# Optimization experiments

Hardware: AMD Instinct MI355X
Metric: run time of the kernel (lower is better)

The kernel has to match this reference:

```python
import jax, jax.numpy as jnp
import numpy as np

N_NODES = 50000


def _sage_max(x, src, dst, W_l, b_l, W_r):
    # gather neighbor (source) features, scatter-max to destination nodes
    msgs = x[src]                                   # [E, F]
    agg = jax.ops.segment_max(msgs, dst, num_segments=N_NODES)  # [N, F], -inf for empty
    agg = jnp.where(jnp.isneginf(agg), 0.0, agg)    # PyG fills isolated nodes with 0
    return agg @ W_l + b_l + x @ W_r                # lin_l(aggr) + lin_r(x)


def setup_inputs() -> dict:
    key = jax.random.key(0)
    ks = jax.random.split(key, 9)
    F_IN, H, OUT, E, EL = 128, 256, 32, 800000, 200000
    x = jax.random.normal(ks[0], (N_NODES, F_IN), dtype=jnp.float32)
    edge_index = jax.random.randint(ks[1], (2, E), 0, N_NODES, dtype=jnp.int64)
    edge_label_index = jax.random.randint(ks[2], (2, EL), 0, N_NODES, dtype=jnp.int64)
    s1 = 1.0 / np.sqrt(F_IN)
    s2 = 1.0 / np.sqrt(H)
    W1_l = jax.random.normal(ks[3], (F_IN, H), dtype=jnp.float32) * s1
    b1 = jnp.zeros((H,), dtype=jnp.float32)
    W1_r = jax.random.normal(ks[4], (F_IN, H), dtype=jnp.float32) * s1
    W2_l = jax.random.normal(ks[5], (H, OUT), dtype=jnp.float32) * s2
    b2 = jnp.zeros((OUT,), dtype=jnp.float32)
    W2_r = jax.random.normal(ks[6], (H, OUT), dtype=jnp.float32) * s2
    return {"x": x, "edge_index": edge_index, "edge_label_index": edge_label_index,
            "W1_l": W1_l, "b1": b1, "W1_r": W1_r,
            "W2_l": W2_l, "b2": b2, "W2_r": W2_r}


def reference(x, edge_index, edge_label_index, W1_l, b1, W1_r, W2_l, b2, W2_r):
    src, dst = edge_index[0], edge_index[1]
    # encode (eval mode: dropout is identity)
    h = jax.nn.relu(_sage_max(x, src, dst, W1_l, b1, W1_r))
    z = _sage_max(h, src, dst, W2_l, b2, W2_r)       # [N, 32]
    # decode: dot product between endpoint embeddings
    s = z[edge_label_index[0]]
    d = z[edge_label_index[1]]
    return jnp.sum(s * d, axis=-1)                   # [E_label]
```

## Files before the change

kernel.cpp:

```cpp
#include <hip/hip_runtime.h>
#include <hip/hip_bf16.h>
#include <math.h>

#define N_NODES 50000
#define NBKT 196
#define BSH 8
#define TILE2 4096
#define CAP 64
#define P2CAP 5888
#define SCAN_FLAG 0x40000000

typedef __attribute__((ext_vector_type(8))) short short8;
typedef __attribute__((ext_vector_type(4))) float f32x4;

static __device__ __forceinline__ float b2f(unsigned int u16) {
    union { unsigned int i; float f; } c; c.i = u16 << 16; return c.f;
}
static __device__ __forceinline__ unsigned int fbits(float f) {
    union { float f; unsigned int i; } c; c.f = f; return c.i;
}
static __device__ __forceinline__ unsigned short f2b_rne(float f) {
    unsigned int u = fbits(f);
    u += 0x7fff + ((u >> 16) & 1);
    return (unsigned short)(u >> 16);
}

static __device__ __forceinline__ unsigned char quant8(float v) {
    int q = (int)(v * 15.9375f + 0.5f);
    return (unsigned char)min(q, 255);
}

static __device__ __forceinline__ short8 dq8(uint2 v8) {
    short8 r;
#pragma unroll
    for (int bi = 0; bi < 4; ++bi)
        r[bi] = (short)f2b_rne((float)((v8.x >> (8 * bi)) & 255u) * 0.0627451f);
#pragma unroll
    for (int bi = 0; bi < 4; ++bi)
        r[4 + bi] = (short)f2b_rne((float)((v8.y >> (8 * bi)) & 255u) * 0.0627451f);
    return r;
}


__global__ __launch_bounds__(256) void k_prepbin(
        const float* __restrict__ x, unsigned short* __restrict__ xb,
        const float* __restrict__ W1l, const float* __restrict__ W1r, unsigned short* __restrict__ wt1,
        const float* __restrict__ W2l, const float* __restrict__ W2r, unsigned short* __restrict__ wt2,
        float* __restrict__ zb,
        const int* __restrict__ src, const int* __restrict__ dst, int E,
        uint2* __restrict__ tmp, int* __restrict__ cnts, int ntile) {
    __shared__ int cnt[256], sstart[256], lcur[256];
    __shared__ uint2 stage[TILE2];
    const int CX = (N_NODES * 128 / 4) / 256;
    const int CW = CX + 320;
    const int CZ = CW + 1563;
    int b = blockIdx.x, t = threadIdx.x;
    if (b < CX) {
        int i = b * 256 + t;
        float4 v = *(const float4*)(x + (size_t)i * 4);
        ushort4 o;
        o.x = f2b_rne(v.x); o.y = f2b_rne(v.y); o.z = f2b_rne(v.z); o.w = f2b_rne(v.w);
        *(ushort4*)(xb + (size_t)i * 4) = o;
    } else if (b < CX + 256) {
        int i = (b - CX) * 256 + t;
        int n = i >> 8, k = i & 255;
        float v = (k < 128) ? W1l[(size_t)k * 256 + n] : W1r[(size_t)(k - 128) * 256 + n];
        wt1[(size_t)n * 256 + k] = f2b_rne(v);
    } else if (b < CW) {
        int i = (b - CX - 256) * 256 + t;
        int n = i >> 9, k = i & 511;
        float v = (k < 256) ? W2l[(size_t)k * 32 + n] : W2r[(size_t)(k - 256) * 32 + n];
        wt2[(size_t)n * 512 + k] = f2b_rne(v);
    } else if (b < CZ) {
        int i = (b - CW) * 256 + t;
        if (i < 400000) ((float4*)zb)[i] = (float4){0.f, 0.f, 0.f, 0.f};
    } else {
        int tb = b - CZ;
        int e0 = tb * TILE2;
        int tilecnt = min(TILE2, E - e0);
        if (tilecnt <= 0) return;
        cnt[t] = 0;
        __syncthreads();
        if (tilecnt == TILE2) {
            for (int i = 4 * t; i < TILE2; i += 1024) {
                int4 d = *(const int4*)(dst + e0 + i);
                atomicAdd(&cnt[d.x >> BSH], 1);
                atomicAdd(&cnt[d.y >> BSH], 1);
                atomicAdd(&cnt[d.z >> BSH], 1);
                atomicAdd(&cnt[d.w >> BSH], 1);
            }
        } else {
            for (int i = t; i < tilecnt; i += 256)
                atomicAdd(&cnt[dst[e0 + i] >> BSH], 1);
        }
        __syncthreads();
        int cv = cnt[t];
        sstart[t] = cv;
        __syncthreads();
        for (int off = 1; off < 256; off <<= 1) {
            int add = (t >= off) ? sstart[t - off] : 0;
            __syncthreads();
            sstart[t] += add;
            __syncthreads();
        }
        int mystart = sstart[t] - cv;
        __syncthreads();
        sstart[t] = mystart;
        lcur[t] = mystart;
        __syncthreads();
        if (tilecnt == TILE2) {
            for (int i = 4 * t; i < TILE2; i += 1024) {
                int4 d = *(const int4*)(dst + e0 + i);
                int4 s = *(const int4*)(src + e0 + i);
                int q0 = atomicAdd(&lcur[d.x >> BSH], 1); stage[q0] = (uint2){(unsigned)s.x, (unsigned)d.x};
                int q1 = atomicAdd(&lcur[d.y >> BSH], 1); stage[q1] = (uint2){(unsigned)s.y, (unsigned)d.y};
                int q2 = atomicAdd(&lcur[d.z >> BSH], 1); stage[q2] = (uint2){(unsigned)s.z, (unsigned)d.z};
                int q3 = atomicAdd(&lcur[d.w >> BSH], 1); stage[q3] = (uint2){(unsigned)s.w, (unsigned)d.w};
            }
        } else {
            for (int i = t; i < tilecnt; i += 256) {
                int d = dst[e0 + i];
                int s = src[e0 + i];
                int q = atomicAdd(&lcur[d >> BSH], 1);
                uint2 p; p.x = (unsigned)s; p.y = (unsigned)d;
                stage[q] = p;
            }
        }
        __syncthreads();
        if (t < NBKT) cnts[(size_t)t * ntile + tb] = cnt[t];
        for (int i = t; i < tilecnt; i += 256) {
            uint2 p = stage[i];
            int bk = (int)(p.y >> BSH);
            tmp[((size_t)bk * ntile + tb) * CAP + (i - sstart[bk])] = p;
        }
    }
}


__global__ __launch_bounds__(256) void k_bin2(const uint2* __restrict__ tmp,
        const int* __restrict__ cnts, int* __restrict__ pub,
        int* __restrict__ rowptr, int* __restrict__ esrc, int N, int E, int ntile) {
    __shared__ int sc[256], toff[260], nodecnt[256], lcur[256];
    __shared__ int stage[P2CAP];
    __shared__ int shsum[4];
    int k = blockIdx.x, t = threadIdx.x;

    int c = (t < ntile) ? cnts[(size_t)k * ntile + t] : 0;
    sc[t] = c;
    __syncthreads();
    for (int off = 1; off < 256; off <<= 1) {
        int add = (t >= off) ? sc[t - off] : 0;
        __syncthreads();
        sc[t] += add;
        __syncthreads();
    }
    if (t < ntile) toff[t] = sc[t] - c;
    if (t == 255) toff[ntile] = sc[255];
    __syncthreads();
    int total = toff[ntile];

    if (t == 255) atomicExch(&pub[k], SCAN_FLAG | total);
    int v = 0;
    if (t < k) {
        int val;
        do { val = atomicOr(&pub[t], 0); } while (!(val & SCAN_FLAG) || (val & 0x80000000));
        v = val & (SCAN_FLAG - 1);
    }
#pragma unroll
    for (int off = 32; off >= 1; off >>= 1) v += __shfl_xor(v, off);
    if ((t & 63) == 0) shsum[t >> 6] = v;
    nodecnt[t] = 0;
    __syncthreads();
    int base = shsum[0] + shsum[1] + shsum[2] + shsum[3];

    for (int i = t; i < total; i += 256) {
        int lo = 0, hi = ntile;
        while (hi - lo > 1) { int mid = (lo + hi) >> 1; if (toff[mid] <= i) lo = mid; else hi = mid; }
        uint2 p = tmp[((size_t)k * ntile + lo) * CAP + (i - toff[lo])];
        atomicAdd(&nodecnt[(int)p.y & 255], 1);
    }
    __syncthreads();

    int nc = nodecnt[t];
    sc[t] = nc;
    __syncthreads();
    for (int off = 1; off < 256; off <<= 1) {
        int add = (t >= off) ? sc[t - off] : 0;
        __syncthreads();
        sc[t] += add;
        __syncthreads();
    }
    int ex = sc[t] - nc;
    int node = (k << BSH) + t;
    if (node < N) rowptr[node] = base + ex;
    if (node == N) rowptr[N] = E;
    lcur[t] = ex;
    __syncthreads();

    if (total <= P2CAP) {
        for (int i = t; i < total; i += 256) {
            int lo = 0, hi = ntile;
            while (hi - lo > 1) { int mid = (lo + hi) >> 1; if (toff[mid] <= i) lo = mid; else hi = mid; }
            uint2 p = tmp[((size_t)k * ntile + lo) * CAP + (i - toff[lo])];
            int q = atomicAdd(&lcur[(int)p.y & 255], 1);
            stage[q] = (int)p.x;
        }
        __syncthreads();
        for (int i = t; i < total; i += 256)
            esrc[base + i] = stage[i];
    } else {
        for (int i = t; i < total; i += 256) {
            int lo = 0, hi = ntile;
            while (hi - lo > 1) { int mid = (lo + hi) >> 1; if (toff[mid] <= i) lo = mid; else hi = mid; }
            uint2 p = tmp[((size_t)k * ntile + lo) * CAP + (i - toff[lo])];
            int q = atomicAdd(&lcur[(int)p.y & 255], 1);
            esrc[base + q] = (int)p.x;
        }
    }
}


__global__ __launch_bounds__(256) void k_seg_max1(const unsigned short* __restrict__ feat,
        const int* __restrict__ rowptr, const int* __restrict__ esrc,
        unsigned short* __restrict__ out) {
    int w = threadIdx.x >> 6, t = threadIdx.x & 63;
    int n = blockIdx.x * 4 + w;
    int lane16 = t & 15, sub = t >> 4;
    int beg = rowptr[n], end = rowptr[n + 1];
    float m[8];
#pragma unroll
    for (int k = 0; k < 8; ++k) m[k] = -INFINITY;
    for (int base = beg; base < end; base += 64) {
        int cnt = min(64, end - base);
        int vidx = (base + t < end) ? __builtin_nontemporal_load(&esrc[base + t]) : 0;
        for (int j = 0; j < cnt; j += 16) {
            uint4 v[4];
#pragma unroll
            for (int u = 0; u < 4; ++u) {
                int e = min(j + 4 * u + sub, cnt - 1);
                int s = __shfl(vidx, e);
                v[u] = *(const uint4*)(feat + (size_t)s * 128 + lane16 * 8);
            }
#pragma unroll
            for (int u = 0; u < 4; ++u) {
                m[0] = fmaxf(m[0], b2f(v[u].x & 0xffff));
                m[1] = fmaxf(m[1], b2f(v[u].x >> 16));
                m[2] = fmaxf(m[2], b2f(v[u].y & 0xffff));
                m[3] = fmaxf(m[3], b2f(v[u].y >> 16));
                m[4] = fmaxf(m[4], b2f(v[u].z & 0xffff));
                m[5] = fmaxf(m[5], b2f(v[u].z >> 16));
                m[6] = fmaxf(m[6], b2f(v[u].w & 0xffff));
                m[7] = fmaxf(m[7], b2f(v[u].w >> 16));
            }
        }
    }
#pragma unroll
    for (int k = 0; k < 8; ++k) {
        m[k] = fmaxf(m[k], __shfl_xor(m[k], 16));
        m[k] = fmaxf(m[k], __shfl_xor(m[k], 32));
        if (beg == end) m[k] = 0.f;
    }
    if (sub == 0) {
        uint4 p;
        p.x = (fbits(m[0]) >> 16) | (fbits(m[1]) & 0xffff0000u);
        p.y = (fbits(m[2]) >> 16) | (fbits(m[3]) & 0xffff0000u);
        p.z = (fbits(m[4]) >> 16) | (fbits(m[5]) & 0xffff0000u);
        p.w = (fbits(m[6]) >> 16) | (fbits(m[7]) & 0xffff0000u);
        *(uint4*)(out + (size_t)n * 128 + lane16 * 8) = p;
    }
}


__global__ __launch_bounds__(256) void k_seg_max2(const unsigned char* __restrict__ feat8,
        const int* __restrict__ rowptr, const int* __restrict__ esrc,
        unsigned char* __restrict__ out8) {
    int w = threadIdx.x >> 6, t = threadIdx.x & 63;
    int n = blockIdx.x * 4 + w;
    int lane16 = t & 15, sub = t >> 4;
    int beg = rowptr[n], end = rowptr[n + 1];
    int m[16];
#pragma unroll
    for (int k = 0; k < 16; ++k) m[k] = 0;
    for (int base = beg; base < end; base += 64) {
        int cnt = min(64, end - base);
        int vidx = (base + t < end) ? __builtin_nontemporal_load(&esrc[base + t]) : 0;
        for (int j = 0; j < cnt; j += 32) {
            uint4 v[8];
#pragma unroll
            for (int u = 0; u < 8; ++u) {
                int e = min(j + 4 * u + sub, cnt - 1);
                int s = __shfl(vidx, e);
                v[u] = *(const uint4*)(feat8 + (size_t)s * 256 + lane16 * 16);
            }
#pragma unroll
            for (int u = 0; u < 8; ++u) {
                m[0]  = max(m[0],  (int)(v[u].x & 0xFF));
                m[1]  = max(m[1],  (int)((v[u].x >> 8) & 0xFF));
                m[2]  = max(m[2],  (int)((v[u].x >> 16) & 0xFF));
                m[3]  = max(m[3],  (int)(v[u].x >> 24));
                m[4]  = max(m[4],  (int)(v[u].y & 0xFF));
                m[5]  = max(m[5],  (int)((v[u].y >> 8) & 0xFF));
                m[6]  = max(m[6],  (int)((v[u].y >> 16) & 0xFF));
                m[7]  = max(m[7],  (int)(v[u].y >> 24));
                m[8]  = max(m[8],  (int)(v[u].z & 0xFF));
                m[9]  = max(m[9],  (int)((v[u].z >> 8) & 0xFF));
                m[10] = max(m[10], (int)((v[u].z >> 16) & 0xFF));
                m[11] = max(m[11], (int)(v[u].z >> 24));
                m[12] = max(m[12], (int)(v[u].w & 0xFF));
                m[13] = max(m[13], (int)((v[u].w >> 8) & 0xFF));
                m[14] = max(m[14], (int)((v[u].w >> 16) & 0xFF));
                m[15] = max(m[15], (int)(v[u].w >> 24));
            }
        }
    }
#pragma unroll
    for (int k = 0; k < 16; ++k) {
        m[k] = max(m[k], __shfl_xor(m[k], 16));
        m[k] = max(m[k], __shfl_xor(m[k], 32));
    }
    if (sub == 0) {
        uint4 p;
        p.x = m[0]  | (m[1]  << 8) | (m[2]  << 16) | (m[3]  << 24);
        p.y = m[4]  | (m[5]  << 8) | (m[6]  << 16) | (m[7]  << 24);
        p.z = m[8]  | (m[9]  << 8) | (m[10] << 16) | (m[11] << 24);
        p.w = m[12] | (m[13] << 8) | (m[14] << 16) | (m[15] << 24);
        *(uint4*)(out8 + (size_t)n * 256 + lane16 * 16) = p;
    }
}


#define STAGE1(Asb, Bsb, K0) do {                                                     \
    const unsigned short* Ab_ = ((K0) < 128) ? A0 : A1;                               \
    int kab_ = ((K0) & 127) * 2;                                                      \
    int kbb_ = (K0) * 2;                                                              \
    _Pragma("unroll")                                                                 \
    for (int ii = 0; ii < 2; ++ii) {                                                  \
        int c_ = ii * 256 + tid;                                                      \
        int r_ = c_ >> 2, gs_ = (c_ & 3) ^ (r_ & 3);                                  \
        const char* ga_ = (const char*)Ab_ + (size_t)(m0 + r_) * 256 + kab_ + gs_ * 16; \
        __builtin_amdgcn_global_load_lds(                                             \
            (const __attribute__((address_space(1))) void*)ga_,                       \
            (__attribute__((address_space(3))) void*)((char*)(Asb) + (ii * 256 + (tid & ~63)) * 16), \
            16, 0, 0);                                                                \
        const char* gb_ = (const char*)WT + (size_t)(n0 + r_) * 512 + kbb_ + gs_ * 16; \
        __builtin_amdgcn_global_load_lds(                                             \
            (const __attribute__((address_space(1))) void*)gb_,                       \
            (__attribute__((address_space(3))) void*)((char*)(Bsb) + (ii * 256 + (tid & ~63)) * 16), \
            16, 0, 0);                                                                \
    }                                                                                 \
} while (0)

__global__ __launch_bounds__(256) void k_lin1_mfma(
        const unsigned short* __restrict__ A0, const unsigned short* __restrict__ A1,
        const unsigned short* __restrict__ WT, const float* __restrict__ bias,
        const unsigned short* __restrict__ WT2, float* __restrict__ zpart,
        unsigned char* __restrict__ H8, int M) {
    __shared__ __align__(16) short SH[17408];
    short* As0 = SH;
    short* As1 = SH + 4096;
    short* Bs0 = SH + 8192;
    short* Bs1 = SH + 12288;
    short* Hs  = SH;

    int tid = threadIdx.x;
    int m0 = blockIdx.y * 128, n0 = blockIdx.x * 128;
    int L = tid & 63, wv = tid >> 6;
    int wr = wv >> 1, wc = wv & 1;
    int lane16 = L & 15, q = L >> 4;

    f32x4 acc[4][4];
#pragma unroll
    for (int i = 0; i < 4; ++i)
#pragma unroll
        for (int j = 0; j < 4; ++j) acc[i][j] = (f32x4){0.f, 0.f, 0.f, 0.f};

    STAGE1(As0, Bs0, 0);
    __syncthreads();

#pragma unroll
    for (int t = 0; t < 8; ++t) {
        const short* Asb = (t & 1) ? As1 : As0;
        const short* Bsb = (t & 1) ? Bs1 : Bs0;
        short* Asn = (t & 1) ? As0 : As1;
        short* Bsn = (t & 1) ? Bs0 : Bs1;
        if (t < 7) STAGE1(Asn, Bsn, (t + 1) * 32);

        short8 a[4], b[4];
#pragma unroll
        for (int i = 0; i < 4; ++i) {
            int r = wr * 64 + i * 16 + lane16;
            a[i] = *(const short8*)((const char*)Asb + r * 64 + ((q ^ (r & 3)) << 4));
        }
#pragma unroll
        for (int j = 0; j < 4; ++j) {
            int c = wc * 64 + j * 16 + lane16;
            b[j] = *(const short8*)((const char*)Bsb + c * 64 + ((q ^ (c & 3)) << 4));
        }
#pragma unroll
        for (int i = 0; i < 4; ++i)
#pragma unroll
            for (int j = 0; j < 4; ++j)
                acc[i][j] = __builtin_amdgcn_mfma_f32_16x16x32_bf16(a[i], b[j], acc[i][j], 0, 0, 0);
        __syncthreads();
    }

#pragma unroll
    for (int i = 0; i < 4; ++i) {
#pragma unroll
        for (int r = 0; r < 4; ++r) {
            int lrow = wr * 64 + i * 16 + q * 4 + r;
            int row = m0 + lrow;
#pragma unroll
            for (int j = 0; j < 4; ++j) {
                int lcol = wc * 64 + j * 16 + lane16;
                int col = n0 + lcol;
                float v = fmaxf(acc[i][j][r] + bias[col], 0.f);
                Hs[lrow * 136 + lcol] = (short)f2b_rne(v);
                if (row < M) H8[(size_t)row * 256 + col] = quant8(v);
            }
        }
    }
    __syncthreads();

    f32x4 acc2[2][2];
#pragma unroll
    for (int i = 0; i < 2; ++i)
#pragma unroll
        for (int j = 0; j < 2; ++j) acc2[i][j] = (f32x4){0.f, 0.f, 0.f, 0.f};
#pragma unroll
    for (int kk = 0; kk < 4; ++kk) {
        short8 a2[2], b2[2];
#pragma unroll
        for (int i = 0; i < 2; ++i)
            a2[i] = *(const short8*)&Hs[(wv * 32 + i * 16 + lane16) * 136 + kk * 32 + q * 8];
#pragma unroll
        for (int j = 0; j < 2; ++j)
            b2[j] = *(const short8*)(WT2 + (size_t)(j * 16 + lane16) * 512 + 256 + n0 + kk * 32 + q * 8);
#pragma unroll
        for (int i = 0; i < 2; ++i)
#pragma unroll
            for (int j = 0; j < 2; ++j)
                acc2[i][j] = __builtin_amdgcn_mfma_f32_16x16x32_bf16(a2[i], b2[j], acc2[i][j], 0, 0, 0);
    }
#pragma unroll
    for (int i = 0; i < 2; ++i) {
#pragma unroll
        for (int r = 0; r < 4; ++r) {
            int row = m0 + wv * 32 + i * 16 + q * 4 + r;
            if (row >= M) continue;
#pragma unroll
            for (int j = 0; j < 2; ++j) {
                int col = j * 16 + lane16;
                atomicAdd(&zpart[(size_t)row * 32 + col], acc2[i][j][r]);
            }
        }
    }
}


#define LD_FRAGS2(RA, BB0, BB1, K0) do {                                              \
    RA = aok0 ? *(const uint2*)(A8 + (size_t)arow0 * 256 + (K0) + q * 8)              \
              : (uint2){0u, 0u};                                                      \
    BB0 = *(const short8*)(WT + (size_t)lane16 * 512 + (K0) + q * 8);                 \
    BB1 = *(const short8*)(WT + (size_t)(16 + lane16) * 512 + (K0) + q * 8);          \
} while (0)

#define DO_MFMA2(RA, BB0, BB1) do {                                                   \
    short8 a_ = dq8(RA);                                                              \
    acc0 = __builtin_amdgcn_mfma_f32_16x16x32_bf16(a_, BB0, acc0, 0, 0, 0);           \
    acc1 = __builtin_amdgcn_mfma_f32_16x16x32_bf16(a_, BB1, acc1, 0, 0, 0);           \
} while (0)

__global__ __launch_bounds__(256) void k_lin2_mfma(
        const unsigned char* __restrict__ A8,
        const unsigned short* __restrict__ WT, const float* __restrict__ bias,
        float* __restrict__ Z, int M) {
    int tid = threadIdx.x;
    int m0 = blockIdx.x * 64;
    int L = tid & 63, wv = tid >> 6;
    int lane16 = L & 15, q = L >> 4;

    f32x4 acc0 = (f32x4){0.f, 0.f, 0.f, 0.f};
    f32x4 acc1 = (f32x4){0.f, 0.f, 0.f, 0.f};

    int arow0 = m0 + wv * 16 + lane16;
    bool aok0 = arow0 < M;

    uint2 xra, yra;
    short8 xb0, xb1, yb0, yb1;
    LD_FRAGS2(xra, xb0, xb1, 0);
    LD_FRAGS2(yra, yb0, yb1, 32);
    DO_MFMA2(xra, xb0, xb1);
    LD_FRAGS2(xra, xb0, xb1, 64);
    DO_MFMA2(yra, yb0, yb1);
    LD_FRAGS2(yra, yb0, yb1, 96);
    DO_MFMA2(xra, xb0, xb1);
    LD_FRAGS2(xra, xb0, xb1, 128);
    DO_MFMA2(yra, yb0, yb1);
    LD_FRAGS2(yra, yb0, yb1, 160);
    DO_MFMA2(xra, xb0, xb1);
    LD_FRAGS2(xra, xb0, xb1, 192);
    DO_MFMA2(yra, yb0, yb1);
    LD_FRAGS2(yra, yb0, yb1, 224);
    DO_MFMA2(xra, xb0, xb1);
    DO_MFMA2(yra, yb0, yb1);

#pragma unroll
    for (int r = 0; r < 4; ++r) {
        int row = m0 + wv * 16 + q * 4 + r;
        if (row >= M) continue;
#pragma unroll
        for (int j = 0; j < 2; ++j) {
            int col = j * 16 + lane16;
            float av = (j == 0) ? acc0[r] : acc1[r];
            float zp = Z[(size_t)row * 32 + col];
            Z[(size_t)row * 32 + col] = av + bias[col] + zp;
        }
    }
}


__global__ void k_decode(const float* __restrict__ z, const int* __restrict__ eli,
                         int EL, float* __restrict__ out) {
    int tid = blockIdx.x * blockDim.x + threadIdx.x;
    int e = tid >> 3, lane = tid & 7;
    if (e >= EL) return;
    int s = eli[e], d = eli[EL + e];
    float4 a = *((const float4*)(z + (size_t)s * 32) + lane);
    float4 b = *((const float4*)(z + (size_t)d * 32) + lane);
    float dot = a.x * b.x + a.y * b.y + a.z * b.z + a.w * b.w;
    dot += __shfl_xor(dot, 1);
    dot += __shfl_xor(dot, 2);
    dot += __shfl_xor(dot, 4);
    if (lane == 0) out[e] = dot;
}


extern "C" void kernel_launch(void* const* d_in, const int* in_sizes, int n_in,
                              void* d_out, int out_size, void* d_ws, size_t ws_size,
                              hipStream_t stream) {
    const float* x   = (const float*)d_in[0];
    const int*   ei  = (const int*)d_in[1];
    const int*   eli = (const int*)d_in[2];
    const float* W1l = (const float*)d_in[3];
    const float* b1  = (const float*)d_in[4];
    const float* W1r = (const float*)d_in[5];
    const float* W2l = (const float*)d_in[6];
    const float* b2  = (const float*)d_in[7];
    const float* W2r = (const float*)d_in[8];
    float* out = (float*)d_out;

    int N  = N_NODES;
    int E  = in_sizes[1] / 2;
    int EL = in_sizes[2] / 2;
    const int* src = ei;
    const int* dst = ei + E;

    char* ws = (char*)d_ws;
    size_t off = 0;
    auto alloc = [&](size_t bytes) -> void* {
        void* p = ws + off;
        off += (bytes + 255) & ~(size_t)255;
        return p;
    };
    unsigned short* xb   = (unsigned short*)alloc((size_t)N * 128 * 2);
    unsigned short* aggb = (unsigned short*)alloc((size_t)(N + 128) * 256 * 2);
    unsigned char*  h8   = (unsigned char*)alloc((size_t)N * 256);
    float* zbuf          = (float*)alloc((size_t)N * 32 * 4);
    unsigned short* wt1  = (unsigned short*)alloc(256 * 256 * 2);
    unsigned short* wt2  = (unsigned short*)alloc(32 * 512 * 2);
    int* rowptr   = (int*)alloc((size_t)(N + 1) * 4);
    int ntile     = (E + TILE2 - 1) / TILE2;
    int* cnts     = (int*)alloc((size_t)NBKT * ntile * 4);
    int* pub      = (int*)alloc(256 * 4);
    int* esrc     = (int*)alloc((size_t)E * 4);
    uint2* tmpp   = (uint2*)aggb;
    unsigned char* agg8 = (unsigned char*)aggb;

    const int tb = 256;
    const int CZ = 6250 + 320 + 1563;

    k_prepbin<<<CZ + ntile, tb, 0, stream>>>(x, xb, W1l, W1r, wt1, W2l, W2r, wt2, zbuf,
                                             src, dst, E, tmpp, cnts, ntile);
    k_bin2<<<NBKT, tb, 0, stream>>>(tmpp, cnts, pub, rowptr, esrc, N, E, ntile);

    k_seg_max1<<<(N + 3) / 4, tb, 0, stream>>>(xb, rowptr, esrc, aggb);
    dim3 g1(2, (N + 127) / 128);
    k_lin1_mfma<<<g1, tb, 0, stream>>>(aggb, xb, wt1, b1, wt2, zbuf, h8, N);

    k_seg_max2<<<(N + 3) / 4, tb, 0, stream>>>(h8, rowptr, esrc, agg8);
    k_lin2_mfma<<<(N + 63) / 64, tb, 0, stream>>>(agg8, wt2, b2, zbuf, N);

    k_decode<<<(EL * 8 + 255) / 256, tb, 0, stream>>>(zbuf, eli, EL, out);
}
```

Before: 245.7 us.

## Triple-buffer lin1 MFMA K-loop with explicit vmcnt waits and barriers

Replaces the double-buffered K loop of the first-layer MFMA GEMM with a three-stage LDS ring. Two tiles are kept in flight, and fine-grained s_waitcnt vmcnt counts replace the full __syncthreads after each step. The goal is to hide global-to-LDS load latency behind MFMA work. In exchange, shared memory grows from 34 KB to 48 KB, which may lower occupancy, and the hand-counted vmcnt values must match the number of loads issued per stage.

```diff
diff --git a/kernel.cpp b/kernel.cpp
--- a/kernel.cpp
+++ b/kernel.cpp
@@ -329,7 +329,7 @@
 }
 
 
-#define STAGE1(Asb, Bsb, K0) do {                                                     \
+#define STAGE(bi, K0) do {                                                            \
     const unsigned short* Ab_ = ((K0) < 128) ? A0 : A1;                               \
     int kab_ = ((K0) & 127) * 2;                                                      \
     int kbb_ = (K0) * 2;                                                              \
@@ -340,14 +340,40 @@
         const char* ga_ = (const char*)Ab_ + (size_t)(m0 + r_) * 256 + kab_ + gs_ * 16; \
         __builtin_amdgcn_global_load_lds(                                             \
             (const __attribute__((address_space(1))) void*)ga_,                       \
-            (__attribute__((address_space(3))) void*)((char*)(Asb) + (ii * 256 + (tid & ~63)) * 16), \
+            (__attribute__((address_space(3))) void*)((char*)(SH + (bi) * 4096) + (ii * 256 + (tid & ~63)) * 16), \
             16, 0, 0);                                                                \
         const char* gb_ = (const char*)WT + (size_t)(n0 + r_) * 512 + kbb_ + gs_ * 16; \
         __builtin_amdgcn_global_load_lds(                                             \
             (const __attribute__((address_space(1))) void*)gb_,                       \
-            (__attribute__((address_space(3))) void*)((char*)(Bsb) + (ii * 256 + (tid & ~63)) * 16), \
+            (__attribute__((address_space(3))) void*)((char*)(SH + 12288 + (bi) * 4096) + (ii * 256 + (tid & ~63)) * 16), \
             16, 0, 0);                                                                \
     }                                                                                 \
+} while (0)
+
+#define VMCNT8() asm volatile("s_waitcnt vmcnt(8)" ::: "memory")
+#define VMCNT4() asm volatile("s_waitcnt vmcnt(4)" ::: "memory")
+#define VMCNT0() asm volatile("s_waitcnt vmcnt(0)" ::: "memory")
+#define SBAR() do { __builtin_amdgcn_sched_barrier(0); __builtin_amdgcn_s_barrier(); __builtin_amdgcn_sched_barrier(0); } while (0)
+
+#define COMPUTE(bi) do {                                                              \
+    const short* Asb_ = SH + (bi) * 4096;                                             \
+    const short* Bsb_ = SH + 12288 + (bi) * 4096;                                     \
+    short8 a_[4], b_[4];                                                              \
+    _Pragma("unroll")                                                                 \
+    for (int i = 0; i < 4; ++i) {                                                     \
+        int r_ = wr * 64 + i * 16 + lane16;                                           \
+        a_[i] = *(const short8*)((const char*)Asb_ + r_ * 64 + ((q ^ (r_ & 3)) << 4)); \
+    }                                                                                 \
+    _Pragma("unroll")                                                                 \
+    for (int j = 0; j < 4; ++j) {                                                     \
+        int c_ = wc * 64 + j * 16 + lane16;                                           \
+        b_[j] = *(const short8*)((const char*)Bsb_ + c_ * 64 + ((q ^ (c_ & 3)) << 4)); \
+    }                                                                                 \
+    _Pragma("unroll")                                                                 \
+    for (int i = 0; i < 4; ++i)                                                       \
+        _Pragma("unroll")                                                             \
+        for (int j = 0; j < 4; ++j)                                                   \
+            acc[i][j] = __builtin_amdgcn_mfma_f32_16x16x32_bf16(a_[i], b_[j], acc[i][j], 0, 0, 0); \
 } while (0)
 
 __global__ __launch_bounds__(256) void k_lin1_mfma(
@@ -355,12 +381,8 @@
         const unsigned short* __restrict__ WT, const float* __restrict__ bias,
         const unsigned short* __restrict__ WT2, float* __restrict__ zpart,
         unsigned char* __restrict__ H8, int M) {
-    __shared__ __align__(16) short SH[17408];
-    short* As0 = SH;
-    short* As1 = SH + 4096;
-    short* Bs0 = SH + 8192;
-    short* Bs1 = SH + 12288;
-    short* Hs  = SH;
+    __shared__ __align__(16) short SH[24576];
+    short* Hs = SH;
 
     int tid = threadIdx.x;
     int m0 = blockIdx.y * 128, n0 = blockIdx.x * 128;
@@ -374,35 +396,20 @@
 #pragma unroll
         for (int j = 0; j < 4; ++j) acc[i][j] = (f32x4){0.f, 0.f, 0.f, 0.f};
 
-    STAGE1(As0, Bs0, 0);
-    __syncthreads();
-
-#pragma unroll
-    for (int t = 0; t < 8; ++t) {
-        const short* Asb = (t & 1) ? As1 : As0;
-        const short* Bsb = (t & 1) ? Bs1 : Bs0;
-        short* Asn = (t & 1) ? As0 : As1;
-        short* Bsn = (t & 1) ? Bs0 : Bs1;
-        if (t < 7) STAGE1(Asn, Bsn, (t + 1) * 32);
-
-        short8 a[4], b[4];
-#pragma unroll
-        for (int i = 0; i < 4; ++i) {
-            int r = wr * 64 + i * 16 + lane16;
-            a[i] = *(const short8*)((const char*)Asb + r * 64 + ((q ^ (r & 3)) << 4));
-        }
-#pragma unroll
-        for (int j = 0; j < 4; ++j) {
-            int c = wc * 64 + j * 16 + lane16;
-            b[j] = *(const short8*)((const char*)Bsb + c * 64 + ((q ^ (c & 3)) << 4));
-        }
-#pragma unroll
-        for (int i = 0; i < 4; ++i)
-#pragma unroll
-            for (int j = 0; j < 4; ++j)
-                acc[i][j] = __builtin_amdgcn_mfma_f32_16x16x32_bf16(a[i], b[j], acc[i][j], 0, 0, 0);
-        __syncthreads();
-    }
+    STAGE(0, 0);
+    STAGE(1, 32);
+    STAGE(2, 64);
+
+    VMCNT8(); SBAR(); COMPUTE(0); SBAR(); STAGE(0, 96);
+    VMCNT8(); SBAR(); COMPUTE(1); SBAR(); STAGE(1, 128);
+    VMCNT8(); SBAR(); COMPUTE(2); SBAR(); STAGE(2, 160);
+    VMCNT8(); SBAR(); COMPUTE(0); SBAR(); STAGE(0, 192);
+    VMCNT8(); SBAR(); COMPUTE(1); SBAR(); STAGE(1, 224);
+    VMCNT8(); SBAR(); COMPUTE(2);
+    VMCNT4(); SBAR(); COMPUTE(0);
+    VMCNT0(); SBAR(); COMPUTE(1);
+
+    __syncthreads();
 
 #pragma unroll
     for (int i = 0; i < 4; ++i) {
```

Result: no change. 244.3 us (-0.6%).
